# Kernel tuning notes

Hardware: AMD Instinct MI355X
Metric: run time of the kernel (lower is better)

## Reference

```python
import jax, jax.numpy as jnp
import numpy as np

THRESHOLD = 0.5


def _crop_resize(img, hstart, ch, wstart, cw, out_h, out_w):
    # Bilinear resample (TF half-pixel-centers) of the crop
    # img[hstart:hstart+ch, wstart:wstart+cw] up to (out_h, out_w).
    chf = ch.astype(jnp.float32)
    cwf = cw.astype(jnp.float32)
    ys = jnp.clip((jnp.arange(out_h, dtype=jnp.float32) + 0.5) * (chf / out_h) - 0.5,
                  0.0, chf - 1.0) + hstart
    xs = jnp.clip((jnp.arange(out_w, dtype=jnp.float32) + 0.5) * (cwf / out_w) - 0.5,
                  0.0, cwf - 1.0) + wstart
    y0 = jnp.floor(ys).astype(jnp.int32)
    y1 = jnp.minimum(y0 + 1, hstart + ch - 1)
    x0 = jnp.floor(xs).astype(jnp.int32)
    x1 = jnp.minimum(x0 + 1, wstart + cw - 1)
    wy = (ys - y0)[:, None, None]
    wx = (xs - x0)[None, :, None]
    r0 = img[y0]  # (out_h, W, C) gathered rows
    r1 = img[y1]
    top = (1.0 - wx) * r0[:, x0] + wx * r0[:, x1]
    bot = (1.0 - wx) * r1[:, x0] + wx * r1[:, x1]
    return (1.0 - wy) * top + wy * bot


def _per_sample(mask, img):
    H, W = img.shape[0], img.shape[1]
    m = (mask >= THRESHOLD).astype(img.dtype)  # (H, W, 1)
    masked = m * img                           # (H, W, C)
    rows = jnp.sum(m[..., 0], axis=1)          # row sums (H,)
    cols = jnp.sum(m[..., 0], axis=0)          # col sums (W,)
    # bbox: first nonzero index - 1 (clamped to 0), last nonzero index + 1
    xl = jnp.maximum(jnp.argmax(rows > 0).astype(jnp.int32) - 1, 0)
    xr = (H - jnp.argmax((rows > 0)[::-1])).astype(jnp.int32)
    yl = jnp.maximum(jnp.argmax(cols > 0).astype(jnp.int32) - 1, 0)
    yr = (W - jnp.argmax((cols > 0)[::-1])).astype(jnp.int32)
    h = xr - xl
    w = yr - yl
    # smart_resize with square target: center-crop bbox to square side min(h, w)
    c = jnp.minimum(h, w)
    hstart = xl + (h - c) // 2
    wstart = yl + (w - c) // 2
    return _crop_resize(masked, hstart, c, wstart, c, H, W)


def setup_inputs() -> dict:
    key = jax.random.key(0)
    k1, k2 = jax.random.split(key)
    masks = jax.random.uniform(k1, (16, 1024, 1024, 1), dtype=jnp.float32)
    images = jax.random.uniform(k2, (16, 1024, 1024, 3), dtype=jnp.float32)
    return {"masks": masks, "images": images}


def reference(masks, images):
    return jax.vmap(_per_sample)(masks, images)
```

## Files before the change

kernel.cpp:

```cpp
#include <hip/hip_runtime.h>

#define HH 1024
#define WW 1024
#define NS 16
#define ROWS_PER_BLOCK 8
#define BLOCKS_X (HH / ROWS_PER_BLOCK)

__global__ __launch_bounds__(256)
void pack_kernel(const float* __restrict__ mask,
                 unsigned int* __restrict__ packed,
                 int* __restrict__ rowMinC,
                 int* __restrict__ rowMaxC) {
    const int s  = blockIdx.y;
    const int r0 = blockIdx.x * ROWS_PER_BLOCK;
    const int t  = threadIdx.x;

    const float4* m4 = (const float4*)(mask + (size_t)s * HH * WW);
    __shared__ int smin[ROWS_PER_BLOCK][4], smax[ROWS_PER_BLOCK][4];

#pragma unroll
    for (int rr = 0; rr < ROWS_PER_BLOCK; ++rr) {
        const int row = r0 + rr;
        float4 v = m4[(size_t)row * 256 + t];
        unsigned int w = (v.x >= 0.5f ? 1u : 0u)
                       | (v.y >= 0.5f ? 2u : 0u)
                       | (v.z >= 0.5f ? 4u : 0u)
                       | (v.w >= 0.5f ? 8u : 0u);
        w |= __shfl_down(w, 1) << 4;
        w |= __shfl_down(w, 2) << 8;
        w |= __shfl_down(w, 4) << 16;

        int cmin = WW, cmax = -1;
        if ((t & 7) == 0) {
            int g = t >> 3;
            packed[((size_t)s * HH + row) * 32 + g] = w;
            if (w) {
                cmin = (g << 5) + __builtin_ctz(w);
                cmax = (g << 5) + 31 - __builtin_clz(w);
            }
        }
        for (int off = 32; off > 0; off >>= 1) {
            cmin = min(cmin, __shfl_down(cmin, off));
            cmax = max(cmax, __shfl_down(cmax, off));
        }
        if ((t & 63) == 0) { smin[rr][t >> 6] = cmin; smax[rr][t >> 6] = cmax; }
    }
    __syncthreads();
    if (t < ROWS_PER_BLOCK) {
        int cmin = min(min(smin[t][0], smin[t][1]), min(smin[t][2], smin[t][3]));
        int cmax = max(max(smax[t][0], smax[t][1]), max(smax[t][2], smax[t][3]));
        rowMinC[s * HH + r0 + t] = cmin;
        rowMaxC[s * HH + r0 + t] = cmax;
    }
}

__global__ __launch_bounds__(256)
void resize_kernel(const float* __restrict__ mask,
                   const float* __restrict__ img,
                   const unsigned int* __restrict__ packed,
                   const int* __restrict__ rowMinC,
                   const int* __restrict__ rowMaxC,
                   float* __restrict__ out) {
    const int s  = blockIdx.y;
    const int r0 = blockIdx.x * ROWS_PER_BLOCK;
    const int t  = threadIdx.x;

    __shared__ unsigned int pw[ROWS_PER_BLOCK][32];
    pw[t >> 5][t & 31] = packed[((size_t)s * HH + r0) * 32 + t];

    int minR = HH, maxR = -1, minC = WW, maxC = -1;
#pragma unroll
    for (int m = 0; m < 4; ++m) {
        int r = t + (m << 8);
        int mc = rowMaxC[s * HH + r];
        if (mc >= 0) {
            minR = min(minR, r);
            maxR = max(maxR, r);
            minC = min(minC, rowMinC[s * HH + r]);
            maxC = max(maxC, mc);
        }
    }
    for (int off = 32; off > 0; off >>= 1) {
        minR = min(minR, __shfl_down(minR, off));
        maxR = max(maxR, __shfl_down(maxR, off));
        minC = min(minC, __shfl_down(minC, off));
        maxC = max(maxC, __shfl_down(maxC, off));
    }
    __shared__ int sm[4][4];
    __shared__ int bc[3];
    int wave = t >> 6, lane = t & 63;
    if (lane == 0) { sm[wave][0] = minR; sm[wave][1] = maxR; sm[wave][2] = minC; sm[wave][3] = maxC; }
    __syncthreads();
    if (t == 0) {
        for (int wv = 1; wv < 4; ++wv) {
            minR = min(minR, sm[wv][0]);
            maxR = max(maxR, sm[wv][1]);
            minC = min(minC, sm[wv][2]);
            maxC = max(maxC, sm[wv][3]);
        }
        int xl, xr, yl, yr;
        if (maxR < 0) { xl = 0; xr = HH; } else { xl = max(minR - 1, 0); xr = maxR + 1; }
        if (maxC < 0) { yl = 0; yr = WW; } else { yl = max(minC - 1, 0); yr = maxC + 1; }
        int h = xr - xl, w = yr - yl;
        int c = min(h, w);
        bc[0] = c;
        bc[1] = xl + (h - c) / 2;
        bc[2] = yl + (w - c) / 2;
    }
    __syncthreads();
    const int c = bc[0], hstart = bc[1], wstart = bc[2];

    const float* im = img + (size_t)s * HH * WW * 3;
    float*      ob  = out + (size_t)s * HH * WW * 3;

    if (c == HH && c == WW && hstart == 0 && wstart == 0) {
        const float4* ip = (const float4*)(im + (size_t)r0 * WW * 3);
        float4*       op = (float4*)(ob + (size_t)r0 * WW * 3);
#pragma unroll
        for (int rr = 0; rr < ROWS_PER_BLOCK; ++rr) {
            const unsigned int* pwr = pw[rr];
#pragma unroll
            for (int j = 0; j < 3; ++j) {
                int fi = t + (j << 8);
                int F  = fi << 2;
                int p0 = F / 3;
                int r  = F - p0 * 3;
                unsigned int b0 = (pwr[p0 >> 5] >> (p0 & 31)) & 1u;
                int p1 = p0 + 1;
                unsigned int b1 = (pwr[p1 >> 5] >> (p1 & 31)) & 1u;
                size_t off = (size_t)rr * 768 + fi;
                float4 v = ip[off];
                float4 o;
                o.x = b0 ? v.x : 0.0f;
                o.y = ((r < 2) ? b0 : b1) ? v.y : 0.0f;
                o.z = ((r == 0) ? b0 : b1) ? v.z : 0.0f;
                o.w = b1 ? v.w : 0.0f;
                op[off] = o;
            }
        }
        return;
    }

    const float* msk = mask + (size_t)s * HH * WW;
    float cf = (float)c;
    float sy = cf / (float)HH;
    float sx = cf / (float)WW;

    for (int rr = 0; rr < ROWS_PER_BLOCK; ++rr) {
        const int row = r0 + rr;
        float ysf = fminf(fmaxf((row + 0.5f) * sy - 0.5f, 0.0f), cf - 1.0f);
        int   y0i = (int)floorf(ysf);
        float wy  = ysf - (float)y0i;
        int   ry0 = hstart + y0i;
        int   ry1 = min(ry0 + 1, hstart + c - 1);
        float* orow = ob + (size_t)row * WW * 3;

        for (int k = 0; k < 4; ++k) {
            int ox = (t << 2) + k;
            float xsf = fminf(fmaxf((ox + 0.5f) * sx - 0.5f, 0.0f), cf - 1.0f);
            int   x0i = (int)floorf(xsf);
            float wx  = xsf - (float)x0i;
            int   rx0 = wstart + x0i;
            int   rx1 = min(rx0 + 1, wstart + c - 1);

            float p00[3], p01[3], p10[3], p11[3];
            auto fetch = [&](int y, int x, float* p) {
                int idx = y * WW + x;
                float mv = msk[idx];
                if (mv >= 0.5f) {
                    const float* q = im + (size_t)idx * 3;
                    p[0] = q[0]; p[1] = q[1]; p[2] = q[2];
                } else {
                    p[0] = 0.0f; p[1] = 0.0f; p[2] = 0.0f;
                }
            };
            fetch(ry0, rx0, p00);
            fetch(ry0, rx1, p01);
            fetch(ry1, rx0, p10);
            fetch(ry1, rx1, p11);

            float* o = orow + (size_t)ox * 3;
#pragma unroll
            for (int ch = 0; ch < 3; ++ch) {
                float top = (1.0f - wx) * p00[ch] + wx * p01[ch];
                float bot = (1.0f - wx) * p10[ch] + wx * p11[ch];
                o[ch] = (1.0f - wy) * top + wy * bot;
            }
        }
    }
}

extern "C" void kernel_launch(void* const* d_in, const int* in_sizes, int n_in,
                              void* d_out, int out_size, void* d_ws, size_t ws_size,
                              hipStream_t stream) {
    const float* masks  = (const float*)d_in[0];
    const float* images = (const float*)d_in[1];
    float* out = (float*)d_out;

    int* rowMinC     = (int*)d_ws;
    int* rowMaxC     = rowMinC + NS * HH;
    unsigned int* pk = (unsigned int*)(rowMaxC + NS * HH);

    pack_kernel  <<<dim3(BLOCKS_X, NS), 256, 0, stream>>>(masks, pk, rowMinC, rowMaxC);
    resize_kernel<<<dim3(BLOCKS_X, NS), 256, 0, stream>>>(masks, images, pk, rowMinC, rowMaxC, out);
}
```

Measured before the change: 100.3 us.

## Hoist bbox reduction into separate kernel, use nontemporal loads/stores, shrink row tiles

Moves the per-sample bounding-box reduction out of the resize kernel into a small dedicated kernel, so each resize block no longer rereads all 1024 row extents. Pack and resize blocks now cover 4 rows instead of 8, giving more blocks. Mask and image streams use nontemporal loads and stores to avoid polluting cache. This costs one extra kernel launch and serializes on the tiny reduce kernel.

```diff
diff --git a/kernel.cpp b/kernel.cpp
--- a/kernel.cpp
+++ b/kernel.cpp
@@ -3,8 +3,10 @@
 #define HH 1024
 #define WW 1024
 #define NS 16
-#define ROWS_PER_BLOCK 8
-#define BLOCKS_X (HH / ROWS_PER_BLOCK)
+#define PR 4
+#define RB 4
+
+typedef float f32x4 __attribute__((ext_vector_type(4)));
 
 __global__ __launch_bounds__(256)
 void pack_kernel(const float* __restrict__ mask,
@@ -12,16 +14,15 @@
                  int* __restrict__ rowMinC,
                  int* __restrict__ rowMaxC) {
     const int s  = blockIdx.y;
-    const int r0 = blockIdx.x * ROWS_PER_BLOCK;
+    const int r0 = blockIdx.x * PR;
     const int t  = threadIdx.x;
 
-    const float4* m4 = (const float4*)(mask + (size_t)s * HH * WW);
-    __shared__ int smin[ROWS_PER_BLOCK][4], smax[ROWS_PER_BLOCK][4];
-
-#pragma unroll
-    for (int rr = 0; rr < ROWS_PER_BLOCK; ++rr) {
+    const f32x4* m4 = (const f32x4*)(mask + (size_t)s * HH * WW);
+    __shared__ int smin[PR][4], smax[PR][4];
+
+    for (int rr = 0; rr < PR; ++rr) {
         const int row = r0 + rr;
-        float4 v = m4[(size_t)row * 256 + t];
+        f32x4 v = __builtin_nontemporal_load(&m4[(size_t)row * 256 + t]);
         unsigned int w = (v.x >= 0.5f ? 1u : 0u)
                        | (v.y >= 0.5f ? 2u : 0u)
                        | (v.z >= 0.5f ? 4u : 0u)
@@ -46,7 +47,7 @@
         if ((t & 63) == 0) { smin[rr][t >> 6] = cmin; smax[rr][t >> 6] = cmax; }
     }
     __syncthreads();
-    if (t < ROWS_PER_BLOCK) {
+    if (t < PR) {
         int cmin = min(min(smin[t][0], smin[t][1]), min(smin[t][2], smin[t][3]));
         int cmax = max(max(smax[t][0], smax[t][1]), max(smax[t][2], smax[t][3]));
         rowMinC[s * HH + r0 + t] = cmin;
@@ -55,22 +56,14 @@
 }
 
 __global__ __launch_bounds__(256)
-void resize_kernel(const float* __restrict__ mask,
-                   const float* __restrict__ img,
-                   const unsigned int* __restrict__ packed,
-                   const int* __restrict__ rowMinC,
+void reduce_kernel(const int* __restrict__ rowMinC,
                    const int* __restrict__ rowMaxC,
-                   float* __restrict__ out) {
-    const int s  = blockIdx.y;
-    const int r0 = blockIdx.x * ROWS_PER_BLOCK;
-    const int t  = threadIdx.x;
-
-    __shared__ unsigned int pw[ROWS_PER_BLOCK][32];
-    pw[t >> 5][t & 31] = packed[((size_t)s * HH + r0) * 32 + t];
-
+                   int* __restrict__ bc4) {
+    const int s = blockIdx.x;
+    const int t = threadIdx.x;
     int minR = HH, maxR = -1, minC = WW, maxC = -1;
 #pragma unroll
-    for (int m = 0; m < 4; ++m) {
+    for (int m = 0; m < HH / 256; ++m) {
         int r = t + (m << 8);
         int mc = rowMaxC[s * HH + r];
         if (mc >= 0) {
@@ -87,7 +80,6 @@
         maxC = max(maxC, __shfl_down(maxC, off));
     }
     __shared__ int sm[4][4];
-    __shared__ int bc[3];
     int wave = t >> 6, lane = t & 63;
     if (lane == 0) { sm[wave][0] = minR; sm[wave][1] = maxR; sm[wave][2] = minC; sm[wave][3] = maxC; }
     __syncthreads();
@@ -103,21 +95,38 @@
         if (maxC < 0) { yl = 0; yr = WW; } else { yl = max(minC - 1, 0); yr = maxC + 1; }
         int h = xr - xl, w = yr - yl;
         int c = min(h, w);
-        bc[0] = c;
-        bc[1] = xl + (h - c) / 2;
-        bc[2] = yl + (w - c) / 2;
-    }
+        bc4[s * 4 + 0] = c;
+        bc4[s * 4 + 1] = xl + (h - c) / 2;
+        bc4[s * 4 + 2] = yl + (w - c) / 2;
+        bc4[s * 4 + 3] = 0;
+    }
+}
+
+__global__ __launch_bounds__(256)
+void resize_kernel(const float* __restrict__ mask,
+                   const float* __restrict__ img,
+                   const unsigned int* __restrict__ packed,
+                   const int* __restrict__ bc4,
+                   float* __restrict__ out) {
+    const int s  = blockIdx.y;
+    const int r0 = blockIdx.x * RB;
+    const int t  = threadIdx.x;
+
+    __shared__ unsigned int pw[RB][32];
+    if (t < RB * 32) pw[t >> 5][t & 31] = packed[((size_t)s * HH + r0) * 32 + t];
+
+    const int c      = bc4[s * 4 + 0];
+    const int hstart = bc4[s * 4 + 1];
+    const int wstart = bc4[s * 4 + 2];
     __syncthreads();
-    const int c = bc[0], hstart = bc[1], wstart = bc[2];
 
     const float* im = img + (size_t)s * HH * WW * 3;
-    float*      ob  = out + (size_t)s * HH * WW * 3;
+    float*       ob = out + (size_t)s * HH * WW * 3;
 
     if (c == HH && c == WW && hstart == 0 && wstart == 0) {
-        const float4* ip = (const float4*)(im + (size_t)r0 * WW * 3);
-        float4*       op = (float4*)(ob + (size_t)r0 * WW * 3);
-#pragma unroll
-        for (int rr = 0; rr < ROWS_PER_BLOCK; ++rr) {
+        const f32x4* ip = (const f32x4*)(im + (size_t)r0 * WW * 3);
+        f32x4*       op = (f32x4*)(ob + (size_t)r0 * WW * 3);
+        for (int rr = 0; rr < RB; ++rr) {
             const unsigned int* pwr = pw[rr];
 #pragma unroll
             for (int j = 0; j < 3; ++j) {
@@ -129,13 +138,13 @@
                 int p1 = p0 + 1;
                 unsigned int b1 = (pwr[p1 >> 5] >> (p1 & 31)) & 1u;
                 size_t off = (size_t)rr * 768 + fi;
-                float4 v = ip[off];
-                float4 o;
+                f32x4 v = __builtin_nontemporal_load(&ip[off]);
+                f32x4 o;
                 o.x = b0 ? v.x : 0.0f;
                 o.y = ((r < 2) ? b0 : b1) ? v.y : 0.0f;
                 o.z = ((r == 0) ? b0 : b1) ? v.z : 0.0f;
                 o.w = b1 ? v.w : 0.0f;
-                op[off] = o;
+                __builtin_nontemporal_store(o, &op[off]);
             }
         }
         return;
@@ -146,7 +155,7 @@
     float sy = cf / (float)HH;
     float sx = cf / (float)WW;
 
-    for (int rr = 0; rr < ROWS_PER_BLOCK; ++rr) {
+    for (int rr = 0; rr < RB; ++rr) {
         const int row = r0 + rr;
         float ysf = fminf(fmaxf((row + 0.5f) * sy - 0.5f, 0.0f), cf - 1.0f);
         int   y0i = (int)floorf(ysf);
@@ -199,8 +208,10 @@
 
     int* rowMinC     = (int*)d_ws;
     int* rowMaxC     = rowMinC + NS * HH;
-    unsigned int* pk = (unsigned int*)(rowMaxC + NS * HH);
-
-    pack_kernel  <<<dim3(BLOCKS_X, NS), 256, 0, stream>>>(masks, pk, rowMinC, rowMaxC);
-    resize_kernel<<<dim3(BLOCKS_X, NS), 256, 0, stream>>>(masks, images, pk, rowMinC, rowMaxC, out);
-}
+    int* bc4         = rowMaxC + NS * HH;
+    unsigned int* pk = (unsigned int*)(bc4 + NS * 4);
+
+    pack_kernel  <<<dim3(HH / PR, NS), 256, 0, stream>>>(masks, pk, rowMinC, rowMaxC);
+    reduce_kernel<<<NS,                256, 0, stream>>>(rowMinC, rowMaxC, bc4);
+    resize_kernel<<<dim3(HH / RB, NS), 256, 0, stream>>>(masks, images, pk, bc4, out);
+}
```

Result: faster. 93.03 us (-7.3%).
